# Optimization experiments

Measured on AMD Instinct MI355X. Metric: run time of the kernel, lower is better.

The kernel has to match this reference:

```python
import jax, jax.numpy as jnp
import numpy as np
from jax import lax

EPS = 1e-12  # torch F.normalize eps


def _unfold3(x):
    # x: [B,C,H,W] -> [B, C*9, H*W]; matches torch F.unfold(k=3, stride=1, pad=1)
    # channel ordering (c, kh, kw), i.e. index = c*9 + kh*3 + kw
    B, C, H, W = x.shape
    xp = jnp.pad(x, ((0, 0), (0, 0), (1, 1), (1, 1)))
    pats = jnp.stack([xp[:, :, i:i + H, j:j + W] for i in range(3) for j in range(3)], axis=2)  # [B,C,9,H,W]
    return pats.reshape(B, C * 9, H * W)


def _fold3(u, H, W):
    # inverse of _unfold3 with overlap-add (torch F.fold, k=3, stride=1, pad=1)
    B, CK, L = u.shape
    C = CK // 9
    u = u.reshape(B, C, 3, 3, H, W)
    canvas = jnp.zeros((B, C, H + 2, W + 2), u.dtype)
    for i in range(3):
        for j in range(3):
            canvas = canvas.at[:, :, i:i + H, j:j + W].add(u[:, :, i, j])
    return canvas[:, :, 1:H + 1, 1:W + 1]


def setup_inputs() -> dict:
    key = jax.random.key(0)
    k1, k2, k3, k4, k5, k6 = jax.random.split(key, 6)
    B, C, H, W = 4, 64, 64, 64
    lr = jax.random.normal(k1, (B, C, H, W), dtype=jnp.float32)
    ref = jax.random.normal(k2, (B, C, H, W), dtype=jnp.float32)
    # fusion: Conv2d(2C, C, 1) then depthwise Conv2d(C, C, 3, groups=C), both with bias
    w1 = jax.random.normal(k3, (C, 2 * C, 1, 1), dtype=jnp.float32) * 0.05
    b1 = jax.random.normal(k4, (C,), dtype=jnp.float32) * 0.05
    wd = jax.random.normal(k5, (C, 1, 3, 3), dtype=jnp.float32) * 0.05
    bd = jax.random.normal(k6, (C,), dtype=jnp.float32) * 0.05
    return {"lr": lr, "ref": ref, "w1": w1, "b1": b1, "wd": wd, "bd": bd}


def reference(lr, ref, w1, b1, wd, bd):
    B, C, H, W = ref.shape
    ref_u = _unfold3(ref)          # [B, 9C, L]
    lr_u = _unfold3(lr)            # [B, 9C, L]
    ref_t = ref_u.transpose(0, 2, 1)  # [B, L, 9C]
    ref_n = ref_t / jnp.maximum(jnp.linalg.norm(ref_t, axis=2, keepdims=True), EPS)
    lr_n = lr_u / jnp.maximum(jnp.linalg.norm(lr_u, axis=1, keepdims=True), EPS)
    R = jnp.einsum('bld,bdm->blm', ref_n, lr_n)  # [B, L, L] cosine correlation
    arg = jnp.argmax(R, axis=1)                  # [B, L] best ref patch per lr position
    T_u = jnp.take_along_axis(ref_u, jnp.broadcast_to(arg[:, None, :], ref_u.shape), axis=2)
    T = _fold3(T_u, H, W)                        # [B, C, H, W]
    x = jnp.concatenate([lr, T], axis=1)         # [B, 2C, H, W]
    dn = ('NCHW', 'OIHW', 'NCHW')
    y = lax.conv_general_dilated(x, w1, (1, 1), 'VALID', dimension_numbers=dn) + b1[None, :, None, None]
    y = lax.conv_general_dilated(y, wd, (1, 1), ((1, 1), (1, 1)), dimension_numbers=dn,
                                 feature_group_count=C) + bd[None, :, None, None]
    return jax.nn.relu(y)
```

## Files before the change

kernel.cpp:

```cpp
#include <hip/hip_runtime.h>
#include <cstdint>
#include <cstddef>


#define BATCH 4
#define CCH 64
#define LPIX 4096
typedef unsigned long long u64;

__device__ __forceinline__ u64 packKey(float v, int idx) {
    unsigned int bits = __float_as_uint(v);
    unsigned int m = (bits & 0x80000000u) ? ~bits : (bits | 0x80000000u);
    return ((u64)m << 32) | (unsigned int)(~(unsigned int)idx);
}

__global__ __launch_bounds__(256) void prep_kernel(const float* __restrict__ ref,
                                                   float* __restrict__ refT,
                                                   float* __restrict__ ssq) {
    __shared__ float s[64 * 65];
    __shared__ float part[256];
    int pt = blockIdx.x, b = blockIdx.y, tid = threadIdx.x;
    const float* rb = ref + ((size_t)b * CCH) * LPIX + pt * 64;
    for (int k = 0; k < 16; ++k) {
        int n = tid + 256 * k;
        int c = n >> 6, p = n & 63;
        s[c * 65 + p] = rb[(size_t)c * LPIX + p];
    }
    __syncthreads();
    {
        int p = tid & 63, g = tid >> 6;
        float acc = 0.f;
        for (int c = g * 16; c < g * 16 + 16; ++c) { float v = s[c * 65 + p]; acc += v * v; }
        part[g * 64 + p] = acc;
    }
    __syncthreads();
    if (tid < 64) {
        float v = part[tid] + part[64 + tid] + part[128 + tid] + part[192 + tid];
        ssq[b * LPIX + pt * 64 + tid] = v;
    }
    float* tb = refT + ((size_t)b * LPIX + pt * 64) * 64;
    for (int k = 0; k < 16; ++k) {
        int n = tid + 256 * k;
        int p = n >> 6, c = n & 63;
        tb[n] = s[c * 65 + p];
    }
}

__global__ __launch_bounds__(256) void invnorm_kernel(const float* __restrict__ ssq,
                                                      float* __restrict__ inv) {
    int t = blockIdx.x * 256 + threadIdx.x;
    int b = t >> 12, p = t & 4095;
    int y = p >> 6, x = p & 63;
    const float* sb = ssq + b * LPIX;
    float n2 = 0.f;
    for (int i = -1; i <= 1; ++i)
        for (int j = -1; j <= 1; ++j) {
            int yy = y + i, xx = x + j;
            if (yy >= 0 && yy < 64 && xx >= 0 && xx < 64) n2 += sb[yy * 64 + xx];
        }
    inv[t] = 1.0f / fmaxf(sqrtf(n2), 1e-12f);
}

__global__ __launch_bounds__(256) void gemmE_kernel(const float* __restrict__ ref,
                                                    const float* __restrict__ lr,
                                                    float* __restrict__ E) {
    __shared__ __align__(16) float sbuf[8192];
    float* As = sbuf;
    float* Bs = sbuf + 4096;
    int r2 = blockIdx.x, r1 = blockIdx.y, b = blockIdx.z, tid = threadIdx.x;
    const float* A = ref + (size_t)b * CCH * LPIX + r1 * 64;
    const float* Bp = lr + (size_t)b * CCH * LPIX + r2 * 64;
    for (int k = 0; k < 4; ++k) {
        int n = tid + 256 * k;
        int c = n >> 4, q = n & 15;
        *(float4*)&As[c * 64 + 4 * q] = *(const float4*)&A[(size_t)c * LPIX + 4 * q];
        *(float4*)&Bs[c * 64 + 4 * q] = *(const float4*)&Bp[(size_t)c * LPIX + 4 * q];
    }
    __syncthreads();
    int tx = tid & 15, ty = tid >> 4;
    float acc[4][4] = {};
#pragma unroll 8
    for (int k = 0; k < 64; ++k) {
        float4 a4 = *(const float4*)&As[k * 64 + 4 * ty];
        float4 b4 = *(const float4*)&Bs[k * 64 + 4 * tx];
        float a[4] = {a4.x, a4.y, a4.z, a4.w};
        float bb[4] = {b4.x, b4.y, b4.z, b4.w};
#pragma unroll
        for (int i = 0; i < 4; ++i)
#pragma unroll
            for (int j = 0; j < 4; ++j) acc[i][j] = fmaf(a[i], bb[j], acc[i][j]);
    }
    __syncthreads();
    float* Dp = sbuf;
    for (int n = tid; n < 66 * 68; n += 256) Dp[n] = 0.f;
    __syncthreads();
#pragma unroll
    for (int i = 0; i < 4; ++i)
#pragma unroll
        for (int j = 0; j < 4; ++j)
            Dp[(4 * ty + i + 1) * 68 + (4 * tx + j + 1)] = acc[i][j];
    __syncthreads();
    float* Et = E + ((size_t)b << 24) + ((size_t)((r1 << 6) + r2) << 12);
#pragma unroll
    for (int i = 0; i < 4; ++i) {
        int r = 4 * ty + i;
        float4 o;
        int c = 4 * tx;
        o.x = Dp[r * 68 + c + 0] + Dp[(r + 1) * 68 + c + 1] + Dp[(r + 2) * 68 + c + 2];
        o.y = Dp[r * 68 + c + 1] + Dp[(r + 1) * 68 + c + 2] + Dp[(r + 2) * 68 + c + 3];
        o.z = Dp[r * 68 + c + 2] + Dp[(r + 1) * 68 + c + 3] + Dp[(r + 2) * 68 + c + 4];
        o.w = Dp[r * 68 + c + 3] + Dp[(r + 1) * 68 + c + 4] + Dp[(r + 2) * 68 + c + 5];
        *(float4*)&Et[r * 64 + c] = o;
    }
}

__global__ __launch_bounds__(256) void band_kernel(const float* __restrict__ E,
                                                   const float* __restrict__ inv,
                                                   u64* __restrict__ packed) {
    __shared__ u64 red[16 * 65];
    int b = blockIdx.z;
    int k = (int)blockIdx.y - 63;
    int t_lo = k < 0 ? -k : 0;
    int t_hi = 64 - (k > 0 ? k : 0);
    int y0 = t_lo + (int)blockIdx.x * 16;
    if (y0 >= t_hi) return;
    int y1 = y0 + 16 < t_hi ? y0 + 16 : t_hi;
    const float* Ebase = E + ((size_t)b << 24);
    const float* invb = inv + b * LPIX;
    u64* pkb = packed + (size_t)b * LPIX;
    int tid = threadIdx.x;
    int c4 = tid & 15, s = tid >> 4;

    float4 Ea[4], Eb[4], Ec[4];
    auto LOADT = [&](float4* T, int t) {
        if (t >= t_lo && t < t_hi) {
            const float4* tp = (const float4*)(Ebase + ((size_t)(((t + k) << 6) + t) << 12));
#pragma unroll
            for (int i = 0; i < 4; ++i) T[i] = tp[tid + 256 * i];
        } else {
#pragma unroll
            for (int i = 0; i < 4; ++i) T[i] = make_float4(0.f, 0.f, 0.f, 0.f);
        }
    };
    LOADT(Ea, y0 - 1); LOADT(Eb, y0); LOADT(Ec, y0 + 1);

    for (int y = y0; y < y1; ++y) {
        int yprow = (y + k) << 6;
        u64 kc0 = 0, kc1 = 0, kc2 = 0, kc3 = 0;
#pragma unroll
        for (int i = 0; i < 4; ++i) {
            int xr = s + 16 * i;
            float iv = invb[yprow + xr];
            int idx = yprow + xr;
            float vx = (Ea[i].x + Eb[i].x + Ec[i].x) * iv;
            float vy = (Ea[i].y + Eb[i].y + Ec[i].y) * iv;
            float vz = (Ea[i].z + Eb[i].z + Ec[i].z) * iv;
            float vw = (Ea[i].w + Eb[i].w + Ec[i].w) * iv;
            u64 t0 = packKey(vx, idx); kc0 = kc0 > t0 ? kc0 : t0;
            u64 t1 = packKey(vy, idx); kc1 = kc1 > t1 ? kc1 : t1;
            u64 t2 = packKey(vz, idx); kc2 = kc2 > t2 ? kc2 : t2;
            u64 t3 = packKey(vw, idx); kc3 = kc3 > t3 ? kc3 : t3;
        }
        red[s * 65 + 4 * c4 + 0] = kc0;
        red[s * 65 + 4 * c4 + 1] = kc1;
        red[s * 65 + 4 * c4 + 2] = kc2;
        red[s * 65 + 4 * c4 + 3] = kc3;
        __syncthreads();
        if (tid < 64) {
            u64 m = red[tid];
#pragma unroll
            for (int ss = 1; ss < 16; ++ss) {
                u64 v = red[ss * 65 + tid];
                m = m > v ? m : v;
            }
            atomicMax(&pkb[(y << 6) + tid], m);
        }
        __syncthreads();
        if (y + 1 < y1) {
            float4 En[4];
            LOADT(En, y + 2);
#pragma unroll
            for (int i = 0; i < 4; ++i) { Ea[i] = Eb[i]; Eb[i] = Ec[i]; Ec[i] = En[i]; }
        }
    }
}

__global__ __launch_bounds__(256) void gather_kernel(const u64* __restrict__ packed,
                                                     const float* __restrict__ refT,
                                                     float* __restrict__ Tt) {
    int b = blockIdx.y;
    int wave = threadIdx.x >> 6, lane = threadIdx.x & 63;
    int p = blockIdx.x * 4 + wave;
    int py = p >> 6, px = p & 63;
    const u64* pk = packed + (size_t)b * LPIX;
    const float* rT = refT + (size_t)b * LPIX * 64;
    float acc = 0.f;
#pragma unroll
    for (int i = 0; i < 3; ++i)
#pragma unroll
        for (int j = 0; j < 3; ++j) {
            int qy = py + 1 - i, qx = px + 1 - j;
            if ((unsigned)qy >= 64u || (unsigned)qx >= 64u) continue;
            int aidx = (int)(~(unsigned int)pk[qy * 64 + qx]);
            int ry = (aidx >> 6) + i - 1, rx = (aidx & 63) + j - 1;
            if ((unsigned)ry >= 64u || (unsigned)rx >= 64u) continue;
            acc += rT[(size_t)(ry * 64 + rx) * 64 + lane];
        }
    Tt[((size_t)b * LPIX + p) * 64 + lane] = acc;
}

#define XST 36
__global__ __launch_bounds__(256) void conv1_kernel(const float* __restrict__ lr,
                                                    const float* __restrict__ Tt,
                                                    const float* __restrict__ w1,
                                                    const float* __restrict__ b1,
                                                    float* __restrict__ z) {
    __shared__ __align__(16) float xs[128 * XST];
    __shared__ __align__(16) float wsm[64 * 128];
    int pt = blockIdx.x, b = blockIdx.y, tid = threadIdx.x;
    for (int k = 0; k < 8; ++k) {
        int n = tid + 256 * k;
        *(float4*)&wsm[4 * n] = *(const float4*)&w1[4 * n];
    }
    const float* lrb = lr + (size_t)b * CCH * LPIX + pt * 32;
    for (int k = 0; k < 2; ++k) {
        int n = tid + 256 * k;
        int c = n >> 3, q = n & 7;
        *(float4*)&xs[c * XST + 4 * q] = *(const float4*)&lrb[(size_t)c * LPIX + 4 * q];
    }
    const float* Tb = Tt + ((size_t)b * LPIX + pt * 32) * 64;
    for (int k = 0; k < 2; ++k) {
        int n = tid + 256 * k;
        int p = n >> 4, cq = n & 15;
        float4 v = *(const float4*)&Tb[p * 64 + 4 * cq];
        xs[(64 + 4 * cq + 0) * XST + p] = v.x;
        xs[(64 + 4 * cq + 1) * XST + p] = v.y;
        xs[(64 + 4 * cq + 2) * XST + p] = v.z;
        xs[(64 + 4 * cq + 3) * XST + p] = v.w;
    }
    __syncthreads();
    int p = tid & 31, g = tid >> 5;
    float acc[8];
#pragma unroll
    for (int t = 0; t < 8; ++t) acc[t] = b1[g * 8 + t];
    for (int c = 0; c < 128; ++c) {
        float xv = xs[c * XST + p];
#pragma unroll
        for (int t = 0; t < 8; ++t) acc[t] = fmaf(wsm[(g * 8 + t) * 128 + c], xv, acc[t]);
    }
    float* zb = z + (size_t)b * CCH * LPIX + pt * 32;
#pragma unroll
    for (int t = 0; t < 8; ++t) zb[(size_t)(g * 8 + t) * LPIX + p] = acc[t];
}

__global__ __launch_bounds__(256) void dw_kernel(const float* __restrict__ z,
                                                 const float* __restrict__ wd,
                                                 const float* __restrict__ bd,
                                                 float* __restrict__ out) {
    __shared__ __align__(16) float zs[4096];
    int c = blockIdx.x, b = blockIdx.y, tid = threadIdx.x;
    const float* zb = z + ((size_t)b * CCH + c) * LPIX;
    for (int k = 0; k < 4; ++k) {
        int n = tid + 256 * k;
        *(float4*)&zs[4 * n] = *(const float4*)&zb[4 * n];
    }
    __syncthreads();
    float w[9];
#pragma unroll
    for (int t = 0; t < 9; ++t) w[t] = wd[c * 9 + t];
    float bias = bd[c];
    float* ob = out + ((size_t)b * CCH + c) * LPIX;
    for (int s = 0; s < 16; ++s) {
        int p = tid + 256 * s;
        int y = p >> 6, x = p & 63;
        float acc = bias;
#pragma unroll
        for (int i = 0; i < 3; ++i) {
            int yy = y + i - 1;
            if ((unsigned)yy >= 64u) continue;
#pragma unroll
            for (int j = 0; j < 3; ++j) {
                int xx = x + j - 1;
                if ((unsigned)xx >= 64u) continue;
                acc = fmaf(zs[yy * 64 + xx], w[i * 3 + j], acc);
            }
        }
        ob[p] = fmaxf(acc, 0.f);
    }
}

extern "C" void kernel_launch(void* const* d_in, const int* in_sizes, int n_in,
                              void* d_out, int out_size, void* d_ws, size_t ws_size,
                              hipStream_t stream) {
    const float* lr  = (const float*)d_in[0];
    const float* ref = (const float*)d_in[1];
    const float* w1  = (const float*)d_in[2];
    const float* b1  = (const float*)d_in[3];
    const float* wd  = (const float*)d_in[4];
    const float* bd  = (const float*)d_in[5];
    float* out = (float*)d_out;

    float* ws = (float*)d_ws;
    float* refT = ws;
    float* ssq  = refT + (size_t)1048576;
    float* inv  = ssq + 16384;
    u64* packed = (u64*)(inv + 16384);
    float* Tt = (float*)(packed + 16384);
    float* z  = Tt + (size_t)1048576;
    float* E  = z + (size_t)1048576;

    int full = (ws_size >= (size_t)12845056 + 4ull * 67108864ull) ? 1 : 0;

    hipMemsetAsync(packed, 0, (size_t)BATCH * LPIX * sizeof(u64), stream);
    prep_kernel<<<dim3(64, BATCH), 256, 0, stream>>>(ref, refT, ssq);
    invnorm_kernel<<<dim3(64), 256, 0, stream>>>(ssq, inv);
    if (full) {
        gemmE_kernel<<<dim3(64, 64, BATCH), 256, 0, stream>>>(ref, lr, E);
        band_kernel<<<dim3(4, 127, BATCH), 256, 0, stream>>>(E, inv, packed);
    } else {
        for (int b = 0; b < BATCH; ++b) {
            gemmE_kernel<<<dim3(64, 64, 1), 256, 0, stream>>>(
                ref + (size_t)b * CCH * LPIX, lr + (size_t)b * CCH * LPIX, E);
            band_kernel<<<dim3(4, 127, 1), 256, 0, stream>>>(
                E, inv + (size_t)b * LPIX, packed + (size_t)b * LPIX);
        }
    }
    gather_kernel<<<dim3(1024, BATCH), 256, 0, stream>>>(packed, refT, Tt);
    conv1_kernel<<<dim3(128, BATCH), 256, 0, stream>>>(lr, Tt, w1, b1, z);
    dw_kernel<<<dim3(64, BATCH), 256, 0, stream>>>(z, wd, bd, out);
}
```

Baseline: 308.5 us.

## Enlarge gemmE tiles to 8x8 per thread and do diagonal sums via shuffles

Each block of the gemmE kernel now computes four 64x64 row-pair tiles, one per wavefront, with an 8x8 register tile per thread instead of 4x4. The previous shared-memory staging for the 3-tap diagonal sum is replaced by cross-lane shuffles of neighbouring accumulator edges. This raises FMA work per shared load and removes extra syncs and LDS round trips. In exchange it doubles LDS use to 64KB and raises register pressure, with a launch-bounds hint of 2 blocks per CU.

Result: no change. 302.7 us (-1.9%).

```diff
diff --git a/kernel.cpp b/kernel.cpp
--- a/kernel.cpp
+++ b/kernel.cpp
@@ -61,56 +61,70 @@
     inv[t] = 1.0f / fmaxf(sqrtf(n2), 1e-12f);
 }
 
-__global__ __launch_bounds__(256) void gemmE_kernel(const float* __restrict__ ref,
-                                                    const float* __restrict__ lr,
-                                                    float* __restrict__ E) {
-    __shared__ __align__(16) float sbuf[8192];
-    float* As = sbuf;
-    float* Bs = sbuf + 4096;
-    int r2 = blockIdx.x, r1 = blockIdx.y, b = blockIdx.z, tid = threadIdx.x;
-    const float* A = ref + (size_t)b * CCH * LPIX + r1 * 64;
-    const float* Bp = lr + (size_t)b * CCH * LPIX + r2 * 64;
-    for (int k = 0; k < 4; ++k) {
-        int n = tid + 256 * k;
-        int c = n >> 4, q = n & 15;
-        *(float4*)&As[c * 64 + 4 * q] = *(const float4*)&A[(size_t)c * LPIX + 4 * q];
-        *(float4*)&Bs[c * 64 + 4 * q] = *(const float4*)&Bp[(size_t)c * LPIX + 4 * q];
-    }
-    __syncthreads();
-    int tx = tid & 15, ty = tid >> 4;
-    float acc[4][4] = {};
-#pragma unroll 8
+__global__ __launch_bounds__(256, 2) void gemmE_kernel(const float* __restrict__ ref,
+                                                       const float* __restrict__ lr,
+                                                       float* __restrict__ E) {
+    __shared__ __align__(16) float As[2 * 4096];
+    __shared__ __align__(16) float Bs[2 * 4096];
+    int bx = blockIdx.x, by = blockIdx.y, b = blockIdx.z, tid = threadIdx.x;
+    const float* Ab = ref + (size_t)b * CCH * LPIX;
+    const float* Bb = lr + (size_t)b * CCH * LPIX;
+#pragma unroll
+    for (int kk = 0; kk < 8; ++kk) {
+        int n = tid + 256 * kk;
+        int h = n >> 10, c = (n >> 4) & 63, q = n & 15;
+        *(float4*)&As[h * 4096 + c * 64 + 4 * q] =
+            *(const float4*)&Ab[(size_t)c * LPIX + (2 * by + h) * 64 + 4 * q];
+        *(float4*)&Bs[h * 4096 + c * 64 + 4 * q] =
+            *(const float4*)&Bb[(size_t)c * LPIX + (2 * bx + h) * 64 + 4 * q];
+    }
+    __syncthreads();
+    int w = tid >> 6, lane = tid & 63, rg = lane >> 3, cg = lane & 7;
+    const float* Ap = As + (w >> 1) * 4096 + rg * 8;
+    const float* Bp = Bs + (w & 1) * 4096 + cg * 8;
+    float acc[8][8] = {};
+#pragma unroll 4
     for (int k = 0; k < 64; ++k) {
-        float4 a4 = *(const float4*)&As[k * 64 + 4 * ty];
-        float4 b4 = *(const float4*)&Bs[k * 64 + 4 * tx];
-        float a[4] = {a4.x, a4.y, a4.z, a4.w};
-        float bb[4] = {b4.x, b4.y, b4.z, b4.w};
-#pragma unroll
-        for (int i = 0; i < 4; ++i)
-#pragma unroll
-            for (int j = 0; j < 4; ++j) acc[i][j] = fmaf(a[i], bb[j], acc[i][j]);
-    }
-    __syncthreads();
-    float* Dp = sbuf;
-    for (int n = tid; n < 66 * 68; n += 256) Dp[n] = 0.f;
-    __syncthreads();
-#pragma unroll
-    for (int i = 0; i < 4; ++i)
-#pragma unroll
-        for (int j = 0; j < 4; ++j)
-            Dp[(4 * ty + i + 1) * 68 + (4 * tx + j + 1)] = acc[i][j];
-    __syncthreads();
-    float* Et = E + ((size_t)b << 24) + ((size_t)((r1 << 6) + r2) << 12);
-#pragma unroll
-    for (int i = 0; i < 4; ++i) {
-        int r = 4 * ty + i;
-        float4 o;
-        int c = 4 * tx;
-        o.x = Dp[r * 68 + c + 0] + Dp[(r + 1) * 68 + c + 1] + Dp[(r + 2) * 68 + c + 2];
-        o.y = Dp[r * 68 + c + 1] + Dp[(r + 1) * 68 + c + 2] + Dp[(r + 2) * 68 + c + 3];
-        o.z = Dp[r * 68 + c + 2] + Dp[(r + 1) * 68 + c + 3] + Dp[(r + 2) * 68 + c + 4];
-        o.w = Dp[r * 68 + c + 3] + Dp[(r + 1) * 68 + c + 4] + Dp[(r + 2) * 68 + c + 5];
-        *(float4*)&Et[r * 64 + c] = o;
+        float4 a0 = *(const float4*)(Ap + k * 64);
+        float4 a1 = *(const float4*)(Ap + k * 64 + 4);
+        float4 b0 = *(const float4*)(Bp + k * 64);
+        float4 b1 = *(const float4*)(Bp + k * 64 + 4);
+        float av[8] = {a0.x, a0.y, a0.z, a0.w, a1.x, a1.y, a1.z, a1.w};
+        float bv[8] = {b0.x, b0.y, b0.z, b0.w, b1.x, b1.y, b1.z, b1.w};
+#pragma unroll
+        for (int i = 0; i < 8; ++i)
+#pragma unroll
+            for (int j = 0; j < 8; ++j) acc[i][j] = fmaf(av[i], bv[j], acc[i][j]);
+    }
+    float up[7], lf[7], dn[8], rt[8], um, dpc;
+#pragma unroll
+    for (int t = 0; t < 7; ++t) up[t] = __shfl(acc[7][t], lane - 8, 64);
+    um = __shfl(acc[7][7], lane - 9, 64);
+#pragma unroll
+    for (int t = 0; t < 7; ++t) lf[t] = __shfl(acc[t][7], lane - 1, 64);
+#pragma unroll
+    for (int t = 1; t < 8; ++t) dn[t] = __shfl(acc[0][t], lane + 8, 64);
+    dpc = __shfl(acc[0][0], lane + 9, 64);
+#pragma unroll
+    for (int t = 1; t < 8; ++t) rt[t] = __shfl(acc[t][0], lane + 1, 64);
+
+    int r1 = 2 * by + (w >> 1), r2 = 2 * bx + (w & 1);
+    float* Et = E + ((size_t)b << 24) + ((size_t)((r1 << 6) + r2) << 12) + (rg * 8) * 64 + cg * 8;
+    bool rgt = rg > 0, rlt = rg < 7, cgt = cg > 0, clt = cg < 7;
+#pragma unroll
+    for (int i = 0; i < 8; ++i) {
+        float e[8];
+#pragma unroll
+        for (int j = 0; j < 8; ++j) {
+            float dm, dpv;
+            if (i >= 1) dm = (j >= 1) ? acc[i - 1][j - 1] : (cgt ? lf[i - 1] : 0.f);
+            else        dm = rgt ? ((j >= 1) ? up[j - 1] : (cgt ? um : 0.f)) : 0.f;
+            if (i <= 6) dpv = (j <= 6) ? acc[i + 1][j + 1] : (clt ? rt[i + 1] : 0.f);
+            else        dpv = rlt ? ((j <= 6) ? dn[j + 1] : (clt ? dpc : 0.f)) : 0.f;
+            e[j] = dm + acc[i][j] + dpv;
+        }
+        *(float4*)(Et + i * 64)     = make_float4(e[0], e[1], e[2], e[3]);
+        *(float4*)(Et + i * 64 + 4) = make_float4(e[4], e[5], e[6], e[7]);
     }
 }
 
@@ -315,11 +329,11 @@
     prep_kernel<<<dim3(64, BATCH), 256, 0, stream>>>(ref, refT, ssq);
     invnorm_kernel<<<dim3(64), 256, 0, stream>>>(ssq, inv);
     if (full) {
-        gemmE_kernel<<<dim3(64, 64, BATCH), 256, 0, stream>>>(ref, lr, E);
+        gemmE_kernel<<<dim3(32, 32, BATCH), 256, 0, stream>>>(ref, lr, E);
         band_kernel<<<dim3(4, 127, BATCH), 256, 0, stream>>>(E, inv, packed);
     } else {
         for (int b = 0; b < BATCH; ++b) {
-            gemmE_kernel<<<dim3(64, 64, 1), 256, 0, stream>>>(
+            gemmE_kernel<<<dim3(32, 32, 1), 256, 0, stream>>>(
                 ref + (size_t)b * CCH * LPIX, lr + (size_t)b * CCH * LPIX, E);
             band_kernel<<<dim3(4, 127, 1), 256, 0, stream>>>(
                 E, inv + (size_t)b * LPIX, packed + (size_t)b * LPIX);
```
